# Kernel optimization log

Hardware: AMD Instinct MI355X
Metric: run time of the kernel (lower is better)

Reference implementation:

```python
import jax, jax.numpy as jnp
import numpy as np

N, E, NFEAT, NHID, NCLASS = 40000, 640000, 128, 128, 40
LN_EPS = 1e-5
L2_EPS = 1e-12


def layer_norm(x, g, b):
    mu = jnp.mean(x, axis=-1, keepdims=True)
    var = jnp.var(x, axis=-1, keepdims=True)
    return (x - mu) * jax.lax.rsqrt(var + LN_EPS) * g + b


def gcn_conv(x, edge_index, edge_weight, Wl, bl, Wr):
    # lin_l projection then PyG propagate (gather src, weight, scatter-add dst)
    h = x @ Wl.T + bl                                  # [N, out]
    msg = h[edge_index[0]] * edge_weight[:, None]       # [E, out]
    agg = jax.ops.segment_sum(msg, edge_index[1], num_segments=N)
    out = agg + x @ Wr.T                                # root (lin_r, no bias)
    # F.normalize(p=2, dim=-1)
    nrm = jnp.sqrt(jnp.sum(out * out, axis=-1, keepdims=True))
    return out / jnp.maximum(nrm, L2_EPS)


def setup_inputs() -> dict:
    key = jax.random.key(0)
    ks = jax.random.split(key, 12)
    x = jax.random.normal(ks[0], (N, NFEAT), dtype=jnp.float32)
    edge_index = jax.random.randint(ks[1], (2, E), 0, N, dtype=jnp.int64)
    edge_weight = jax.random.uniform(ks[2], (E,), dtype=jnp.float32)
    # kaiming-normal-ish init scales
    s0 = np.sqrt(2.0 / NFEAT)
    s1 = np.sqrt(2.0 / NHID)
    return {
        "x": x,
        "edge_index": edge_index,
        "edge_weight": edge_weight,
        "ln0_g": jnp.ones((NFEAT,), jnp.float32),
        "ln0_b": jnp.zeros((NFEAT,), jnp.float32),
        "W0l": jax.random.normal(ks[3], (NHID, NFEAT), jnp.float32) * s0,
        "b0l": jnp.zeros((NHID,), jnp.float32),
        "W0r": jax.random.normal(ks[4], (NHID, NFEAT), jnp.float32) * s0,
        "ln1_g": jnp.ones((NHID,), jnp.float32),
        "ln1_b": jnp.zeros((NHID,), jnp.float32),
        "W1l": jax.random.normal(ks[5], (NCLASS, NHID), jnp.float32) * s1,
        "b1l": jnp.zeros((NCLASS,), jnp.float32),
        "W1r": jax.random.normal(ks[6], (NCLASS, NHID), jnp.float32) * s1,
    }


def reference(x, edge_index, edge_weight, ln0_g, ln0_b, W0l, b0l, W0r,
              ln1_g, ln1_b, W1l, b1l, W1r):
    # layer_norm_first
    h = layer_norm(x, ln0_g, ln0_b)
    h = gcn_conv(h, edge_index, edge_weight, W0l, b0l, W0r)
    h = layer_norm(h, ln1_g, ln1_b)
    h = jax.nn.relu(h)  # dropout inactive in eval mode
    h = gcn_conv(h, edge_index, edge_weight, W1l, b1l, W1r)
    return jax.nn.log_softmax(h, axis=1)
```

## Files before the change

### kernel.cpp

```cpp
#include <hip/hip_runtime.h>
#include <math.h>

#define N_NODES 40000
#define N_EDGES 640000
#define BCAP 64
#define FGRP 8
#define FRANGE (N_NODES / FGRP)
#define NCHUNK (N_EDGES / 256)
#define NSG 5084

typedef __attribute__((ext_vector_type(8))) short short8;
typedef __attribute__((ext_vector_type(4))) float f32x4;

__device__ __forceinline__ unsigned short f2bf(float f) {
    union { float f; unsigned u; } v; v.f = f;
    unsigned r = (v.u + 0x7FFFu + ((v.u >> 16) & 1u)) >> 16;
    return (unsigned short)r;
}
__device__ __forceinline__ float bf2f(unsigned short h) {
    union { unsigned u; float f; } v; v.u = ((unsigned)h) << 16;
    return v.f;
}

__device__ __forceinline__ float wave_sum(float v) {
    #pragma unroll
    for (int m = 1; m < 64; m <<= 1) v += __shfl_xor(v, m, 64);
    return v;
}
__device__ __forceinline__ float wave_max(float v) {
    #pragma unroll
    for (int m = 1; m < 64; m <<= 1) v = fmaxf(v, __shfl_xor(v, m, 64));
    return v;
}

__global__ __launch_bounds__(256) void comboFill_kernel(const float* __restrict__ x,
        const float* __restrict__ g, const float* __restrict__ b,
        unsigned short* __restrict__ h0h, unsigned short* __restrict__ h0l,
        const float* __restrict__ W0l, const float* __restrict__ W0r,
        const float* __restrict__ W1l, const float* __restrict__ W1r,
        unsigned short* __restrict__ Wt1h, unsigned short* __restrict__ Wt1l,
        unsigned short* __restrict__ Wt2h, unsigned short* __restrict__ Wt2l,
        const int* __restrict__ ei, const float* __restrict__ ew,
        int* __restrict__ cnt, unsigned int* __restrict__ sPk) {
    int bid = blockIdx.x;
    int ph = bid % 3;
    if (ph < 2) {
        int cb = (bid / 3) * 2 + ph;
        if (cb < 10000) {
            int row = cb * 4 + (threadIdx.x >> 6);
            int lane = threadIdx.x & 63;
            float2 v = ((const float2*)(x + (size_t)row * 128))[lane];
            float mu = wave_sum(v.x + v.y) * (1.0f / 128.0f);
            float dx = v.x - mu, dy = v.y - mu;
            float var = wave_sum(dx * dx + dy * dy) * (1.0f / 128.0f);
            float rs = rsqrtf(var + 1e-5f);
            float2 gv = ((const float2*)g)[lane];
            float2 bv = ((const float2*)b)[lane];
            float ox = dx * rs * gv.x + bv.x;
            float oy = dy * rs * gv.y + bv.y;
            ushort2 hv, lv;
            hv.x = f2bf(ox); hv.y = f2bf(oy);
            lv.x = f2bf(ox - bf2f(hv.x)); lv.y = f2bf(oy - bf2f(hv.y));
            ((ushort2*)(h0h + (size_t)row * 128))[lane] = hv;
            ((ushort2*)(h0l + (size_t)row * 128))[lane] = lv;
        } else {
            int i = (cb - 10000) * 256 + threadIdx.x;
            float w; unsigned short *ph2, *pl; int idx;
            if (i < 256 * 128) {
                int c = i >> 7, k = i & 127;
                w = (c < 128) ? W0l[c * 128 + k] : W0r[(c - 128) * 128 + k];
                ph2 = Wt1h; pl = Wt1l; idx = i;
            } else {
                int j = i - 256 * 128;
                int c = j >> 7, k = j & 127;
                w = (c < 40) ? W1l[c * 128 + k] : W1r[(c - 40) * 128 + k];
                ph2 = Wt2h; pl = Wt2l; idx = j;
            }
            unsigned short hi = f2bf(w);
            ph2[idx] = hi;
            pl[idx] = f2bf(w - bf2f(hi));
        }
    } else {
        int gp = bid & 7;
        int j = (bid / 3) >> 3;
        int lo = gp * FRANGE;
        #pragma unroll
        for (int cc = 0; cc < 4; ++cc) {
            int chunk = j * 4 + cc;
            if (chunk < NCHUNK) {
                int e = chunk * 256 + threadIdx.x;
                int d = ei[N_EDGES + e];
                if (d >= lo && d < lo + FRANGE) {
                    unsigned int pk = (unsigned int)ei[e] | ((unsigned int)f2bf(ew[e]) << 16);
                    int rank = atomicAdd(&cnt[d], 1);
                    if (rank < BCAP) sPk[(size_t)d * BCAP + rank] = pk;
                }
            }
        }
    }
}


__global__ __launch_bounds__(256) void gemm1_kernel(
        const unsigned short* __restrict__ h0h, const unsigned short* __restrict__ h0l,
        const unsigned short* __restrict__ Wt1h, const unsigned short* __restrict__ Wt1l,
        const float* __restrict__ b0l,
        unsigned short* __restrict__ hl, unsigned short* __restrict__ agg) {
    __shared__ unsigned short Bs[2][128 * 128];
    int tid = threadIdx.x;
    int cBase = blockIdx.y * 128;
    #pragma unroll
    for (int plane = 0; plane < 2; ++plane) {
        const unsigned short* src = plane ? Wt1l : Wt1h;
        char* dst = (char*)Bs[plane];
        #pragma unroll
        for (int i = 0; i < 8; ++i) {
            int gid = i * 256 + tid;
            int c = gid >> 4, kc = gid & 15;
            short8 v = *(const short8*)(src + (size_t)(cBase + c) * 128 + kc * 8);
            int byte = (c * 256 + kc * 16) ^ ((c & 7) << 4);
            *(short8*)(dst + byte) = v;
        }
    }
    __syncthreads();

    int wid = tid >> 6, lane = tid & 63;
    int rBase = (blockIdx.x * 4 + wid) * 32;
    if (rBase < N_NODES) {
        int lr = lane & 15;
        int lk = (lane >> 4) * 8;
        int sw = (lr & 7) << 4;
        const unsigned short* a0h = h0h + (size_t)(rBase + lr) * 128 + lk;
        const unsigned short* a0l = h0l + (size_t)(rBase + lr) * 128 + lk;
        const unsigned short* a1h = a0h + 16 * 128;
        const unsigned short* a1l = a0l + 16 * 128;
        f32x4 acc[2][8] = {};
        #pragma unroll
        for (int ks = 0; ks < 4; ++ks) {
            int kb = ks * 32;
            short8 A0h = *(const short8*)(a0h + kb);
            short8 A0l = *(const short8*)(a0l + kb);
            short8 A1h = *(const short8*)(a1h + kb);
            short8 A1l = *(const short8*)(a1l + kb);
            #pragma unroll
            for (int ct = 0; ct < 8; ++ct) {
                int bb = (((ct * 16 + lr) << 8) + (ks << 6) + ((lane >> 4) << 4)) ^ sw;
                short8 Bh = *(const short8*)((const char*)Bs[0] + bb);
                short8 Bl = *(const short8*)((const char*)Bs[1] + bb);
                acc[0][ct] = __builtin_amdgcn_mfma_f32_16x16x32_bf16(A0h, Bh, acc[0][ct], 0, 0, 0);
                acc[0][ct] = __builtin_amdgcn_mfma_f32_16x16x32_bf16(A0h, Bl, acc[0][ct], 0, 0, 0);
                acc[0][ct] = __builtin_amdgcn_mfma_f32_16x16x32_bf16(A0l, Bh, acc[0][ct], 0, 0, 0);
                acc[1][ct] = __builtin_amdgcn_mfma_f32_16x16x32_bf16(A1h, Bh, acc[1][ct], 0, 0, 0);
                acc[1][ct] = __builtin_amdgcn_mfma_f32_16x16x32_bf16(A1h, Bl, acc[1][ct], 0, 0, 0);
                acc[1][ct] = __builtin_amdgcn_mfma_f32_16x16x32_bf16(A1l, Bh, acc[1][ct], 0, 0, 0);
            }
        }
        int orow = (lane >> 4) * 4;
        #pragma unroll
        for (int rt = 0; rt < 2; ++rt) {
            int row = rBase + rt * 16 + orow;
            #pragma unroll
            for (int ct = 0; ct < 8; ++ct) {
                int col = cBase + ct * 16 + lr;
                if (col < 128) {
                    float bias = b0l[col];
                    #pragma unroll
                    for (int j = 0; j < 4; ++j)
                        hl[(size_t)(row + j) * 128 + col] = f2bf(acc[rt][ct][j] + bias);
                } else {
                    int cc = col - 128;
                    #pragma unroll
                    for (int j = 0; j < 4; ++j)
                        agg[(size_t)(row + j) * 128 + cc] = f2bf(acc[rt][ct][j]);
                }
            }
        }
    }
}

__global__ __launch_bounds__(256) void gemm2_kernel(
        const unsigned short* __restrict__ h2h, const unsigned short* __restrict__ h2l,
        const unsigned short* __restrict__ Wt2h, const unsigned short* __restrict__ Wt2l,
        const float* __restrict__ b1l,
        unsigned short* __restrict__ gl, unsigned short* __restrict__ agg2) {
    __shared__ unsigned short Bs[2][80 * 128];
    int tid = threadIdx.x;
    #pragma unroll
    for (int plane = 0; plane < 2; ++plane) {
        const unsigned short* src = plane ? Wt2l : Wt2h;
        char* dst = (char*)Bs[plane];
        #pragma unroll
        for (int i = 0; i < 5; ++i) {
            int gid = i * 256 + tid;
            int c = gid >> 4, kc = gid & 15;
            short8 v = *(const short8*)(src + (size_t)c * 128 + kc * 8);
            int byte = (c * 256 + kc * 16) ^ ((c & 7) << 4);
            *(short8*)(dst + byte) = v;
        }
    }
    __syncthreads();

    int wid = tid >> 6, lane = tid & 63;
    int rBase = (blockIdx.x * 4 + wid) * 32;
    if (rBase < N_NODES) {
        int lr = lane & 15;
        int lk = (lane >> 4) * 8;
        int sw = (lr & 7) << 4;
        const unsigned short* a0h = h2h + (size_t)(rBase + lr) * 128 + lk;
        const unsigned short* a0l = h2l + (size_t)(rBase + lr) * 128 + lk;
        const unsigned short* a1h = a0h + 16 * 128;
        const unsigned short* a1l = a0l + 16 * 128;
        f32x4 acc[2][5] = {};
        #pragma unroll
        for (int ks = 0; ks < 4; ++ks) {
            int kb = ks * 32;
            short8 A0h = *(const short8*)(a0h + kb);
            short8 A0l = *(const short8*)(a0l + kb);
            short8 A1h = *(const short8*)(a1h + kb);
            short8 A1l = *(const short8*)(a1l + kb);
            #pragma unroll
            for (int ct = 0; ct < 5; ++ct) {
                int bb = (((ct * 16 + lr) << 8) + (ks << 6) + ((lane >> 4) << 4)) ^ sw;
                short8 Bh = *(const short8*)((const char*)Bs[0] + bb);
                short8 Bl = *(const short8*)((const char*)Bs[1] + bb);
                acc[0][ct] = __builtin_amdgcn_mfma_f32_16x16x32_bf16(A0h, Bh, acc[0][ct], 0, 0, 0);
                acc[0][ct] = __builtin_amdgcn_mfma_f32_16x16x32_bf16(A0h, Bl, acc[0][ct], 0, 0, 0);
                acc[0][ct] = __builtin_amdgcn_mfma_f32_16x16x32_bf16(A0l, Bh, acc[0][ct], 0, 0, 0);
                acc[1][ct] = __builtin_amdgcn_mfma_f32_16x16x32_bf16(A1h, Bh, acc[1][ct], 0, 0, 0);
                acc[1][ct] = __builtin_amdgcn_mfma_f32_16x16x32_bf16(A1h, Bl, acc[1][ct], 0, 0, 0);
                acc[1][ct] = __builtin_amdgcn_mfma_f32_16x16x32_bf16(A1l, Bh, acc[1][ct], 0, 0, 0);
            }
        }
        int orow = (lane >> 4) * 4;
        #pragma unroll
        for (int rt = 0; rt < 2; ++rt) {
            int row = rBase + rt * 16 + orow;
            #pragma unroll
            for (int ct = 0; ct < 5; ++ct) {
                int col = ct * 16 + lr;
                if (col < 40) {
                    float bias = b1l[col];
                    #pragma unroll
                    for (int j = 0; j < 4; ++j)
                        gl[(size_t)(row + j) * 40 + col] = f2bf(acc[rt][ct][j] + bias);
                } else {
                    int cc = col - 40;
                    #pragma unroll
                    for (int j = 0; j < 4; ++j)
                        agg2[(size_t)(row + j) * 40 + cc] = f2bf(acc[rt][ct][j]);
                }
            }
        }
    }
}

__global__ __launch_bounds__(256) void gather1_kernel(const int* __restrict__ cnt,
        const unsigned int* __restrict__ sPk, const unsigned short* __restrict__ hl,
        const unsigned short* __restrict__ agg,
        const float* __restrict__ g, const float* __restrict__ b,
        unsigned short* __restrict__ h2h, unsigned short* __restrict__ h2l) {
    int row = blockIdx.x * 4 + (threadIdx.x >> 6);
    int lane = threadIdx.x & 63;
    int n = cnt[row]; n = n > BCAP ? BCAP : n;
    const unsigned int* ep = sPk + (size_t)row * BCAP;
    ushort2 r0 = ((const ushort2*)(agg + (size_t)row * 128))[lane];
    float2 acc; acc.x = bf2f(r0.x); acc.y = bf2f(r0.y);
    int e = 0;
    for (; e + 8 <= n; e += 8) {
        uint4 q0 = *(const uint4*)(ep + e);
        uint4 q1 = *(const uint4*)(ep + e + 4);
        ushort2 u0 = ((const ushort2*)(hl + (size_t)(q0.x & 0xFFFF) * 128))[lane];
        ushort2 u1 = ((const ushort2*)(hl + (size_t)(q0.y & 0xFFFF) * 128))[lane];
        ushort2 u2 = ((const ushort2*)(hl + (size_t)(q0.z & 0xFFFF) * 128))[lane];
        ushort2 u3 = ((const ushort2*)(hl + (size_t)(q0.w & 0xFFFF) * 128))[lane];
        ushort2 u4 = ((const ushort2*)(hl + (size_t)(q1.x & 0xFFFF) * 128))[lane];
        ushort2 u5 = ((const ushort2*)(hl + (size_t)(q1.y & 0xFFFF) * 128))[lane];
        ushort2 u6 = ((const ushort2*)(hl + (size_t)(q1.z & 0xFFFF) * 128))[lane];
        ushort2 u7 = ((const ushort2*)(hl + (size_t)(q1.w & 0xFFFF) * 128))[lane];
        float w0 = bf2f((unsigned short)(q0.x >> 16)), w1 = bf2f((unsigned short)(q0.y >> 16));
        float w2 = bf2f((unsigned short)(q0.z >> 16)), w3 = bf2f((unsigned short)(q0.w >> 16));
        float w4 = bf2f((unsigned short)(q1.x >> 16)), w5 = bf2f((unsigned short)(q1.y >> 16));
        float w6 = bf2f((unsigned short)(q1.z >> 16)), w7 = bf2f((unsigned short)(q1.w >> 16));
        acc.x = fmaf(bf2f(u0.x), w0, acc.x); acc.y = fmaf(bf2f(u0.y), w0, acc.y);
        acc.x = fmaf(bf2f(u1.x), w1, acc.x); acc.y = fmaf(bf2f(u1.y), w1, acc.y);
        acc.x = fmaf(bf2f(u2.x), w2, acc.x); acc.y = fmaf(bf2f(u2.y), w2, acc.y);
        acc.x = fmaf(bf2f(u3.x), w3, acc.x); acc.y = fmaf(bf2f(u3.y), w3, acc.y);
        acc.x = fmaf(bf2f(u4.x), w4, acc.x); acc.y = fmaf(bf2f(u4.y), w4, acc.y);
        acc.x = fmaf(bf2f(u5.x), w5, acc.x); acc.y = fmaf(bf2f(u5.y), w5, acc.y);
        acc.x = fmaf(bf2f(u6.x), w6, acc.x); acc.y = fmaf(bf2f(u6.y), w6, acc.y);
        acc.x = fmaf(bf2f(u7.x), w7, acc.x); acc.y = fmaf(bf2f(u7.y), w7, acc.y);
    }
    for (; e < n; ++e) {
        unsigned int p = ep[e];
        ushort2 u = ((const ushort2*)(hl + (size_t)(p & 0xFFFF) * 128))[lane];
        float w = bf2f((unsigned short)(p >> 16));
        acc.x = fmaf(bf2f(u.x), w, acc.x);
        acc.y = fmaf(bf2f(u.y), w, acc.y);
    }
    float nrm = sqrtf(wave_sum(acc.x * acc.x + acc.y * acc.y));
    float inv = 1.0f / fmaxf(nrm, 1e-12f);
    float vx = acc.x * inv, vy = acc.y * inv;
    float mu = wave_sum(vx + vy) * (1.0f / 128.0f);
    float dx = vx - mu, dy = vy - mu;
    float var = wave_sum(dx * dx + dy * dy) * (1.0f / 128.0f);
    float rs = rsqrtf(var + 1e-5f);
    float2 gv = ((const float2*)g)[lane];
    float2 bv = ((const float2*)b)[lane];
    float ox = fmaxf(dx * rs * gv.x + bv.x, 0.0f);
    float oy = fmaxf(dy * rs * gv.y + bv.y, 0.0f);
    ushort2 hv, lv;
    hv.x = f2bf(ox); hv.y = f2bf(oy);
    lv.x = f2bf(ox - bf2f(hv.x)); lv.y = f2bf(oy - bf2f(hv.y));
    ((ushort2*)(h2h + (size_t)row * 128))[lane] = hv;
    ((ushort2*)(h2l + (size_t)row * 128))[lane] = lv;
}

__global__ __launch_bounds__(256) void gather2_kernel(const int* __restrict__ cnt,
        const unsigned int* __restrict__ sPk, const unsigned short* __restrict__ gl,
        const unsigned short* __restrict__ agg2, float* __restrict__ out) {
    int row = blockIdx.x * 4 + (threadIdx.x >> 6);
    int lane = threadIdx.x & 63;
    bool act = lane < 40;
    int n = cnt[row]; n = n > BCAP ? BCAP : n;
    const unsigned int* ep = sPk + (size_t)row * BCAP;
    float acc = act ? bf2f(agg2[(size_t)row * 40 + lane]) : 0.0f;
    int e = 0;
    for (; e + 8 <= n; e += 8) {
        uint4 q0 = *(const uint4*)(ep + e);
        uint4 q1 = *(const uint4*)(ep + e + 4);
        if (act) {
            float v0 = bf2f(gl[(size_t)(q0.x & 0xFFFF) * 40 + lane]);
            float v1 = bf2f(gl[(size_t)(q0.y & 0xFFFF) * 40 + lane]);
            float v2 = bf2f(gl[(size_t)(q0.z & 0xFFFF) * 40 + lane]);
            float v3 = bf2f(gl[(size_t)(q0.w & 0xFFFF) * 40 + lane]);
            float v4 = bf2f(gl[(size_t)(q1.x & 0xFFFF) * 40 + lane]);
            float v5 = bf2f(gl[(size_t)(q1.y & 0xFFFF) * 40 + lane]);
            float v6 = bf2f(gl[(size_t)(q1.z & 0xFFFF) * 40 + lane]);
            float v7 = bf2f(gl[(size_t)(q1.w & 0xFFFF) * 40 + lane]);
            acc = fmaf(v0, bf2f((unsigned short)(q0.x >> 16)), acc);
            acc = fmaf(v1, bf2f((unsigned short)(q0.y >> 16)), acc);
            acc = fmaf(v2, bf2f((unsigned short)(q0.z >> 16)), acc);
            acc = fmaf(v3, bf2f((unsigned short)(q0.w >> 16)), acc);
            acc = fmaf(v4, bf2f((unsigned short)(q1.x >> 16)), acc);
            acc = fmaf(v5, bf2f((unsigned short)(q1.y >> 16)), acc);
            acc = fmaf(v6, bf2f((unsigned short)(q1.z >> 16)), acc);
            acc = fmaf(v7, bf2f((unsigned short)(q1.w >> 16)), acc);
        }
    }
    for (; e < n; ++e) {
        unsigned int p = ep[e];
        if (act) {
            float v = bf2f(gl[(size_t)(p & 0xFFFF) * 40 + lane]);
            acc = fmaf(v, bf2f((unsigned short)(p >> 16)), acc);
        }
    }
    float nrm = sqrtf(wave_sum(act ? acc * acc : 0.0f));
    float o = acc / fmaxf(nrm, 1e-12f);
    float m = wave_max(act ? o : -INFINITY);
    float s = wave_sum(act ? expf(o - m) : 0.0f);
    float ls = logf(s);
    if (act) out[(size_t)row * 40 + lane] = o - m - ls;
}

extern "C" void kernel_launch(void* const* d_in, const int* in_sizes, int n_in,
                              void* d_out, int out_size, void* d_ws, size_t ws_size,
                              hipStream_t stream) {
    const float* x    = (const float*)d_in[0];
    const int*   ei   = (const int*)d_in[1];
    const float* ew   = (const float*)d_in[2];
    const float* ln0g = (const float*)d_in[3];
    const float* ln0b = (const float*)d_in[4];
    const float* W0l  = (const float*)d_in[5];
    const float* b0l  = (const float*)d_in[6];
    const float* W0r  = (const float*)d_in[7];
    const float* ln1g = (const float*)d_in[8];
    const float* ln1b = (const float*)d_in[9];
    const float* W1l  = (const float*)d_in[10];
    const float* b1l  = (const float*)d_in[11];
    const float* W1r  = (const float*)d_in[12];
    float* out = (float*)d_out;

    const size_t NBUF = (size_t)N_NODES * 128;
    char* p = (char*)d_ws;
    auto alloc = [&](size_t bytes) { char* r = p; p += (bytes + 255) & ~(size_t)255; return r; };
    unsigned short* agg  = (unsigned short*)alloc(NBUF * 2);
    unsigned short* hl   = (unsigned short*)alloc(NBUF * 2);
    unsigned short* h0h  = (unsigned short*)alloc(NBUF * 2);
    unsigned short* h0l  = (unsigned short*)alloc(NBUF * 2);
    unsigned short* Wt1h = (unsigned short*)alloc(256 * 128 * 2);
    unsigned short* Wt1l = (unsigned short*)alloc(256 * 128 * 2);
    unsigned short* Wt2h = (unsigned short*)alloc(80 * 128 * 2);
    unsigned short* Wt2l = (unsigned short*)alloc(80 * 128 * 2);
    unsigned int*   sPk  = (unsigned int*)alloc((size_t)N_NODES * BCAP * 4);
    int*            cnt  = (int*)alloc(N_NODES * 4);
    unsigned short* gl   = hl;
    unsigned short* agg2 = agg;

    hipMemsetAsync(cnt, 0, (size_t)N_NODES * 4, stream);
    comboFill_kernel<<<NSG * 3, 256, 0, stream>>>(x, ln0g, ln0b, h0h, h0l,
            W0l, W0r, W1l, W1l == W1r ? W1r : W1r, Wt1h, Wt1l, Wt2h, Wt2l, ei, ew, cnt, sPk);
    gemm1_kernel<<<dim3(313, 2), 256, 0, stream>>>(h0h, h0l, Wt1h, Wt1l, b0l, hl, agg);
    gather1_kernel<<<N_NODES / 4, 256, 0, stream>>>(cnt, sPk, hl, agg,
                                                    ln1g, ln1b, h0h, h0l);
    gemm2_kernel<<<313, 256, 0, stream>>>(h0h, h0l, Wt2h, Wt2l, b1l, gl, agg2);
    gather2_kernel<<<N_NODES / 4, 256, 0, stream>>>(cnt, sPk, gl, agg2, out);
}
```

Baseline: 137.2 us.

## Drop low-bf16 split of first-layer activations and remap gather row order

The first LayerNorm output is now stored only as a single bf16 plane, so gemm1 no longer loads an h0l plane and issues two instead of three MFMAs per tile, which cuts the write of a full activation buffer and a third of the first GEMM's matrix work. Separately, both gather kernels remap block indices so that consecutive blocks interleave across the eight FRANGE row ranges used when the edge buckets were filled, changing the order in which nodes are processed and their memory locality. The precision cut reduces accuracy of the first projection to roughly bf16 on the activation side, which may matter for tolerance.

```diff
diff --git a/kernel.cpp b/kernel.cpp
--- a/kernel.cpp
+++ b/kernel.cpp
@@ -35,7 +35,7 @@
 
 __global__ __launch_bounds__(256) void comboFill_kernel(const float* __restrict__ x,
         const float* __restrict__ g, const float* __restrict__ b,
-        unsigned short* __restrict__ h0h, unsigned short* __restrict__ h0l,
+        unsigned short* __restrict__ h0h,
         const float* __restrict__ W0l, const float* __restrict__ W0r,
         const float* __restrict__ W1l, const float* __restrict__ W1r,
         unsigned short* __restrict__ Wt1h, unsigned short* __restrict__ Wt1l,
@@ -56,13 +56,10 @@
             float rs = rsqrtf(var + 1e-5f);
             float2 gv = ((const float2*)g)[lane];
             float2 bv = ((const float2*)b)[lane];
-            float ox = dx * rs * gv.x + bv.x;
-            float oy = dy * rs * gv.y + bv.y;
-            ushort2 hv, lv;
-            hv.x = f2bf(ox); hv.y = f2bf(oy);
-            lv.x = f2bf(ox - bf2f(hv.x)); lv.y = f2bf(oy - bf2f(hv.y));
+            ushort2 hv;
+            hv.x = f2bf(dx * rs * gv.x + bv.x);
+            hv.y = f2bf(dy * rs * gv.y + bv.y);
             ((ushort2*)(h0h + (size_t)row * 128))[lane] = hv;
-            ((ushort2*)(h0l + (size_t)row * 128))[lane] = lv;
         } else {
             int i = (cb - 10000) * 256 + threadIdx.x;
             float w; unsigned short *ph2, *pl; int idx;
@@ -102,7 +99,7 @@
 
 
 __global__ __launch_bounds__(256) void gemm1_kernel(
-        const unsigned short* __restrict__ h0h, const unsigned short* __restrict__ h0l,
+        const unsigned short* __restrict__ h0h,
         const unsigned short* __restrict__ Wt1h, const unsigned short* __restrict__ Wt1l,
         const float* __restrict__ b0l,
         unsigned short* __restrict__ hl, unsigned short* __restrict__ agg) {
@@ -131,17 +128,13 @@
         int lk = (lane >> 4) * 8;
         int sw = (lr & 7) << 4;
         const unsigned short* a0h = h0h + (size_t)(rBase + lr) * 128 + lk;
-        const unsigned short* a0l = h0l + (size_t)(rBase + lr) * 128 + lk;
         const unsigned short* a1h = a0h + 16 * 128;
-        const unsigned short* a1l = a0l + 16 * 128;
         f32x4 acc[2][8] = {};
         #pragma unroll
         for (int ks = 0; ks < 4; ++ks) {
             int kb = ks * 32;
             short8 A0h = *(const short8*)(a0h + kb);
-            short8 A0l = *(const short8*)(a0l + kb);
             short8 A1h = *(const short8*)(a1h + kb);
-            short8 A1l = *(const short8*)(a1l + kb);
             #pragma unroll
             for (int ct = 0; ct < 8; ++ct) {
                 int bb = (((ct * 16 + lr) << 8) + (ks << 6) + ((lane >> 4) << 4)) ^ sw;
@@ -149,10 +142,8 @@
                 short8 Bl = *(const short8*)((const char*)Bs[1] + bb);
                 acc[0][ct] = __builtin_amdgcn_mfma_f32_16x16x32_bf16(A0h, Bh, acc[0][ct], 0, 0, 0);
                 acc[0][ct] = __builtin_amdgcn_mfma_f32_16x16x32_bf16(A0h, Bl, acc[0][ct], 0, 0, 0);
-                acc[0][ct] = __builtin_amdgcn_mfma_f32_16x16x32_bf16(A0l, Bh, acc[0][ct], 0, 0, 0);
                 acc[1][ct] = __builtin_amdgcn_mfma_f32_16x16x32_bf16(A1h, Bh, acc[1][ct], 0, 0, 0);
                 acc[1][ct] = __builtin_amdgcn_mfma_f32_16x16x32_bf16(A1h, Bl, acc[1][ct], 0, 0, 0);
-                acc[1][ct] = __builtin_amdgcn_mfma_f32_16x16x32_bf16(A1l, Bh, acc[1][ct], 0, 0, 0);
             }
         }
         int orow = (lane >> 4) * 4;
@@ -259,7 +250,8 @@
         const unsigned short* __restrict__ agg,
         const float* __restrict__ g, const float* __restrict__ b,
         unsigned short* __restrict__ h2h, unsigned short* __restrict__ h2l) {
-    int row = blockIdx.x * 4 + (threadIdx.x >> 6);
+    int bid = blockIdx.x;
+    int row = (bid & 7) * FRANGE + (bid >> 3) * 4 + (threadIdx.x >> 6);
     int lane = threadIdx.x & 63;
     int n = cnt[row]; n = n > BCAP ? BCAP : n;
     const unsigned int* ep = sPk + (size_t)row * BCAP;
@@ -318,7 +310,8 @@
 __global__ __launch_bounds__(256) void gather2_kernel(const int* __restrict__ cnt,
         const unsigned int* __restrict__ sPk, const unsigned short* __restrict__ gl,
         const unsigned short* __restrict__ agg2, float* __restrict__ out) {
-    int row = blockIdx.x * 4 + (threadIdx.x >> 6);
+    int bid = blockIdx.x;
+    int row = (bid & 7) * FRANGE + (bid >> 3) * 4 + (threadIdx.x >> 6);
     int lane = threadIdx.x & 63;
     bool act = lane < 40;
     int n = cnt[row]; n = n > BCAP ? BCAP : n;
@@ -386,7 +379,7 @@
     unsigned short* agg  = (unsigned short*)alloc(NBUF * 2);
     unsigned short* hl   = (unsigned short*)alloc(NBUF * 2);
     unsigned short* h0h  = (unsigned short*)alloc(NBUF * 2);
-    unsigned short* h0l  = (unsigned short*)alloc(NBUF * 2);
+    unsigned short* h2l  = (unsigned short*)alloc(NBUF * 2);
     unsigned short* Wt1h = (unsigned short*)alloc(256 * 128 * 2);
     unsigned short* Wt1l = (unsigned short*)alloc(256 * 128 * 2);
     unsigned short* Wt2h = (unsigned short*)alloc(80 * 128 * 2);
@@ -397,11 +390,11 @@
     unsigned short* agg2 = agg;
 
     hipMemsetAsync(cnt, 0, (size_t)N_NODES * 4, stream);
-    comboFill_kernel<<<NSG * 3, 256, 0, stream>>>(x, ln0g, ln0b, h0h, h0l,
-            W0l, W0r, W1l, W1l == W1r ? W1r : W1r, Wt1h, Wt1l, Wt2h, Wt2l, ei, ew, cnt, sPk);
-    gemm1_kernel<<<dim3(313, 2), 256, 0, stream>>>(h0h, h0l, Wt1h, Wt1l, b0l, hl, agg);
+    comboFill_kernel<<<NSG * 3, 256, 0, stream>>>(x, ln0g, ln0b, h0h,
+            W0l, W0r, W1l, W1r, Wt1h, Wt1l, Wt2h, Wt2l, ei, ew, cnt, sPk);
+    gemm1_kernel<<<dim3(313, 2), 256, 0, stream>>>(h0h, Wt1h, Wt1l, b0l, hl, agg);
     gather1_kernel<<<N_NODES / 4, 256, 0, stream>>>(cnt, sPk, hl, agg,
-                                                    ln1g, ln1b, h0h, h0l);
-    gemm2_kernel<<<313, 256, 0, stream>>>(h0h, h0l, Wt2h, Wt2l, b1l, gl, agg2);
+                                                    ln1g, ln1b, h0h, h2l);
+    gemm2_kernel<<<313, 256, 0, stream>>>(h0h, h2l, Wt2h, Wt2l, b1l, gl, agg2);
     gather2_kernel<<<N_NODES / 4, 256, 0, stream>>>(cnt, sPk, gl, agg2, out);
 }
```

After: 132.4 us. 3.5% less time.
